# Kernel optimization log

Measured on AMD Instinct MI355X. Metric: run time of the kernel, lower is better.

The kernel has to match this reference:

```python
import jax, jax.numpy as jnp
import numpy as np

N, C, H_IMG, W_IMG = 32, 3, 224, 224
P = 14                      # number_patches per side
PH, PW = H_IMG // P, W_IMG // P
IN_DIM = C * PH * PW        # 768
D = 768                     # hidden_dimension
NH = 12                     # number_heads
DH = D // NH                # 64
L = 12                      # number_blocks
OUT = 1000                  # output_dimension
S = P * P + 1               # 197 tokens (cls + patches)
MLP = 4 * D                 # mlp_ratio * d


def sinusoidal_pos_emb(s, d):
    # result[i][j] = sin(i / 10000^(j/d)) if j even else cos(i / 10000^((j-1)/d))
    i = np.arange(s, dtype=np.float64)[:, None]
    j = np.arange(d)[None, :]
    angle = i / (10000.0 ** ((j - (j % 2)) / float(d)))
    emb = np.where(j % 2 == 0, np.sin(angle), np.cos(angle))
    return jnp.asarray(emb, jnp.float32)


def setup_inputs() -> dict:
    key = jax.random.key(0)
    ks = jax.random.split(key, 12)
    f32 = jnp.float32
    p = {}
    p['images'] = jax.random.normal(ks[0], (N, C, H_IMG, W_IMG), f32)
    p['W_map'] = jax.random.normal(ks[1], (IN_DIM, D), f32) * 0.02
    p['b_map'] = jnp.zeros((D,), f32)
    p['class_token'] = jax.random.normal(ks[2], (1, D), f32)
    p['pos_emb'] = sinusoidal_pos_emb(S, D)  # frozen (requires_grad=False)
    p['ln1_g'] = jnp.ones((L, D), f32)
    p['ln1_b'] = jnp.zeros((L, D), f32)
    p['Wq'] = jax.random.normal(ks[3], (L, NH, DH, DH), f32) * 0.02
    p['bq'] = jnp.zeros((L, NH, DH), f32)
    p['Wk'] = jax.random.normal(ks[4], (L, NH, DH, DH), f32) * 0.02
    p['bk'] = jnp.zeros((L, NH, DH), f32)
    p['Wv'] = jax.random.normal(ks[5], (L, NH, DH, DH), f32) * 0.02
    p['bv'] = jnp.zeros((L, NH, DH), f32)
    p['ln2_g'] = jnp.ones((L, D), f32)
    p['ln2_b'] = jnp.zeros((L, D), f32)
    p['W1'] = jax.random.normal(ks[6], (L, D, MLP), f32) * 0.02
    p['b1'] = jnp.zeros((L, MLP), f32)
    p['W2'] = jax.random.normal(ks[7], (L, MLP, D), f32) * 0.02
    p['b2'] = jnp.zeros((L, D), f32)
    p['W_head'] = jax.random.normal(ks[8], (D, OUT), f32) * 0.02
    p['b_head'] = jnp.zeros((OUT,), f32)
    return p


def _layer_norm(x, g, b, eps=1e-5):
    mu = jnp.mean(x, axis=-1, keepdims=True)
    var = jnp.var(x, axis=-1, keepdims=True)
    return (x - mu) * jax.lax.rsqrt(var + eps) * g + b


def reference(images, W_map, b_map, class_token, pos_emb, ln1_g, ln1_b,
              Wq, bq, Wk, bk, Wv, bv, ln2_g, ln2_b, W1, b1, W2, b2,
              W_head, b_head):
    n = images.shape[0]
    # patchify: [N,C,H,W] -> [N, P*P, C*ph*pw]; per-patch flatten is (C,ph,pw) order
    patches = images.reshape(n, C, P, PH, P, PW)
    patches = patches.transpose(0, 2, 4, 1, 3, 5).reshape(n, P * P, IN_DIM)
    tokens = patches @ W_map + b_map                         # [N, P*P, D]
    cls = jnp.broadcast_to(class_token[None], (n, 1, D))
    x = jnp.concatenate([cls, tokens], axis=1) + pos_emb     # [N, S, D]

    scale = DH ** 0.5
    for l in range(L):
        # --- MHSA with per-head independent Linear weights ---
        h = _layer_norm(x, ln1_g[l], ln1_b[l])
        xh = h.reshape(n, S, NH, DH)
        q = jnp.einsum('nshd,hde->nshe', xh, Wq[l]) + bq[l]
        k = jnp.einsum('nshd,hde->nshe', xh, Wk[l]) + bk[l]
        v = jnp.einsum('nshd,hde->nshe', xh, Wv[l]) + bv[l]
        scores = jnp.einsum('nqhd,nkhd->nhqk', q, k) / scale  # [N,H,S,S]
        attn = jax.nn.softmax(scores, axis=-1)
        o = jnp.einsum('nhqk,nkhd->nqhd', attn, v).reshape(n, S, D)
        x = x + o
        # --- MLP (exact GELU, as torch.nn.GELU default) ---
        h2 = _layer_norm(x, ln2_g[l], ln2_b[l])
        m = jax.nn.gelu(h2 @ W1[l] + b1[l], approximate=False) @ W2[l] + b2[l]
        x = x + m

    logits = x[:, 0] @ W_head + b_head
    return jax.nn.softmax(logits, axis=-1)
```

## Files before the change

kernel.cpp:

```cpp
#include <hip/hip_runtime.h>
#include <hip/hip_bf16.h>

constexpr int N_   = 32;
constexpr int C_   = 3;
constexpr int P_   = 14;
constexpr int PHW  = 16;
constexpr int IND  = 768;
constexpr int D_   = 768;
constexpr int NH_  = 12;
constexpr int DH_  = 64;
constexpr int L_   = 12;
constexpr int OUT_ = 1000;
constexpr int S_   = 197;
constexpr int MLP_ = 3072;
constexpr int NPATCH = P_ * P_;
constexpr int ROWS   = N_ * S_;
constexpr int TROWS  = N_ * NPATCH;
constexpr int RPAD   = 6400;
constexpr int SP_R   = 256;
constexpr int SP_C   = 224;

typedef __attribute__((ext_vector_type(8))) short bf16x8;
typedef __attribute__((ext_vector_type(4))) float f32x4;

__device__ __forceinline__ float bf2f(ushort u) {
    union { float f; unsigned int i; } v; v.i = ((unsigned int)u) << 16; return v.f;
}
__device__ __forceinline__ ushort f2bf(float f) {
    union { float f; unsigned int i; } v; v.f = f;
    unsigned int r = v.i + 0x7fffu + ((v.i >> 16) & 1u);
    return (ushort)(r >> 16);
}

__global__ __launch_bounds__(256)
void mfma_gemm(const ushort* __restrict__ Ag,
               const ushort* __restrict__ Bg,
               void* __restrict__ Cg,
               const float* __restrict__ bias,
               int M, int N, int K,
               int lda, int ldb, int ldc,
               long offA1, long offA2,
               long offB1, long offB2,
               long offC1, long offC2,
               int inner, float alpha, int act, int outbf, int accum)
{
    const int bz = blockIdx.z;
    const int bi = bz / inner, bj = bz % inner;
    const ushort* A = Ag + bi * offA1 + bj * offA2;
    const ushort* B = Bg + bi * offB1 + bj * offB2;
    const long coff = bi * offC1 + bj * offC2;

    __shared__ ushort As[128 * 32];
    __shared__ ushort Bs[128 * 32];

    const int tid  = threadIdx.x;
    const int w    = tid >> 6;
    const int lhi  = (tid & 63) >> 4;
    const int llo  = tid & 15;
    const int wr   = w >> 1, wc = w & 1;
    const int row0 = blockIdx.y * 128;
    const int col0 = blockIdx.x * 128;

    f32x4 acc[4][4];
#pragma unroll
    for (int m = 0; m < 4; ++m)
#pragma unroll
        for (int n = 0; n < 4; ++n) acc[m][n] = (f32x4){0.f, 0.f, 0.f, 0.f};

    int r0s = (0 * 256 + tid) >> 2, s0s = tid & 3;
    int r1s = (1 * 256 + tid) >> 2, s1s = tid & 3;
    int ss0 = s0s ^ ((r0s >> 1) & 3);
    int ss1 = s1s ^ ((r1s >> 1) & 3);
    ushort* dstA0 = As + ((0 * 256 + (w << 6)) << 3);
    ushort* dstA1 = As + ((1 * 256 + (w << 6)) << 3);
    ushort* dstB0 = Bs + ((0 * 256 + (w << 6)) << 3);
    ushort* dstB1 = Bs + ((1 * 256 + (w << 6)) << 3);

    for (int k0 = 0; k0 < K; k0 += 32) {
        const ushort* a0 = A + (long)(row0 + r0s) * lda + k0 + ss0 * 8;
        const ushort* a1 = A + (long)(row0 + r1s) * lda + k0 + ss1 * 8;
        const ushort* b0 = B + (long)(col0 + r0s) * ldb + k0 + ss0 * 8;
        const ushort* b1 = B + (long)(col0 + r1s) * ldb + k0 + ss1 * 8;
        __builtin_amdgcn_global_load_lds((const __attribute__((address_space(1))) void*)a0,
                                         (__attribute__((address_space(3))) void*)dstA0, 16, 0, 0);
        __builtin_amdgcn_global_load_lds((const __attribute__((address_space(1))) void*)a1,
                                         (__attribute__((address_space(3))) void*)dstA1, 16, 0, 0);
        __builtin_amdgcn_global_load_lds((const __attribute__((address_space(1))) void*)b0,
                                         (__attribute__((address_space(3))) void*)dstB0, 16, 0, 0);
        __builtin_amdgcn_global_load_lds((const __attribute__((address_space(1))) void*)b1,
                                         (__attribute__((address_space(3))) void*)dstB1, 16, 0, 0);
        __syncthreads();

        bf16x8 av[4], bv[4];
#pragma unroll
        for (int m = 0; m < 4; ++m) {
            int R = wr * 64 + m * 16 + llo;
            av[m] = *(const bf16x8*)(As + R * 32 + ((lhi ^ ((R >> 1) & 3)) << 3));
        }
#pragma unroll
        for (int n = 0; n < 4; ++n) {
            int R = wc * 64 + n * 16 + llo;
            bv[n] = *(const bf16x8*)(Bs + R * 32 + ((lhi ^ ((R >> 1) & 3)) << 3));
        }
#pragma unroll
        for (int m = 0; m < 4; ++m)
#pragma unroll
            for (int n = 0; n < 4; ++n)
                acc[m][n] = __builtin_amdgcn_mfma_f32_16x16x32_bf16(av[m], bv[n], acc[m][n], 0, 0, 0);
        __syncthreads();
    }

    float* Cf = (float*)Cg + coff;
    ushort* Ch = (ushort*)Cg + coff;
#pragma unroll
    for (int m = 0; m < 4; ++m) {
#pragma unroll
        for (int n = 0; n < 4; ++n) {
#pragma unroll
            for (int j = 0; j < 4; ++j) {
                int gr = row0 + wr * 64 + m * 16 + lhi * 4 + j;
                int gc = col0 + wc * 64 + n * 16 + llo;
                if (gr < M && gc < N) {
                    float v = acc[m][n][j] * alpha;
                    if (bias) v += bias[gc];
                    if (act == 1) v = 0.5f * v * (1.f + erff(v * 0.70710678118654752f));
                    long ci = (long)gr * ldc + gc;
                    if (outbf) {
                        Ch[ci] = f2bf(v);
                    } else {
                        if (accum) v += Cf[ci];
                        Cf[ci] = v;
                    }
                }
            }
        }
    }
}

__global__ __launch_bounds__(256)
void im2col_kernel(const float* __restrict__ img, ushort* __restrict__ patches)
{
    long idx = (long)blockIdx.x * 256 + threadIdx.x;
    if (idx >= (long)TROWS * IND) return;
    int e = (int)(idx % IND);
    int t = (int)((idx / IND) % NPATCH);
    int n = (int)(idx / ((long)IND * NPATCH));
    int pw = e & 15, ph = (e >> 4) & 15, c = e >> 8;
    int px = t % P_, py = t / P_;
    patches[idx] = f2bf(img[(((long)n * C_ + c) * 224 + py * PHW + ph) * 224 + px * PHW + pw]);
}

__global__ __launch_bounds__(256)
void assemble_kernel(const float* __restrict__ tokens,
                     const float* __restrict__ cls,
                     const float* __restrict__ pos,
                     float* __restrict__ x)
{
    long idx = (long)blockIdx.x * 256 + threadIdx.x;
    if (idx >= (long)ROWS * D_) return;
    int d = (int)(idx % D_);
    int s = (int)((idx / D_) % S_);
    long n = idx / ((long)D_ * S_);
    float v = (s == 0) ? cls[d] : tokens[((long)n * NPATCH + (s - 1)) * D_ + d];
    x[idx] = v + pos[(long)s * D_ + d];
}

__global__ __launch_bounds__(256)
void layernorm_kernel(const float* __restrict__ x, ushort* __restrict__ out,
                      const float* __restrict__ g, const float* __restrict__ b)
{
    long row = blockIdx.x;
    const float* xr = x + row * D_;
    ushort* orow = out + row * D_;
    int tid = threadIdx.x;
    float v0 = xr[tid], v1 = xr[tid + 256], v2 = xr[tid + 512];
    float s  = v0 + v1 + v2;
    float sq = v0 * v0 + v1 * v1 + v2 * v2;
    for (int off = 32; off > 0; off >>= 1) {
        s  += __shfl_down(s, off);
        sq += __shfl_down(sq, off);
    }
    __shared__ float rs[4], rq[4];
    int wave = tid >> 6, lane = tid & 63;
    if (lane == 0) { rs[wave] = s; rq[wave] = sq; }
    __syncthreads();
    float S  = rs[0] + rs[1] + rs[2] + rs[3];
    float SQ = rq[0] + rq[1] + rq[2] + rq[3];
    float mean = S * (1.f / 768.f);
    float var  = SQ * (1.f / 768.f) - mean * mean;
    float rstd = rsqrtf(var + 1e-5f);
    orow[tid]       = f2bf((v0 - mean) * rstd * g[tid]       + b[tid]);
    orow[tid + 256] = f2bf((v1 - mean) * rstd * g[tid + 256] + b[tid + 256]);
    orow[tid + 512] = f2bf((v2 - mean) * rstd * g[tid + 512] + b[tid + 512]);
}

__global__ __launch_bounds__(64)
void softmax197_kernel(ushort* __restrict__ scores)
{
    long bid = blockIdx.x;
    long batch = bid / S_;
    long r = bid % S_;
    ushort* p = scores + (batch * SP_R + r) * SP_C;
    int lane = threadIdx.x;
    float v[4];
    float mx = -INFINITY;
#pragma unroll
    for (int i = 0; i < 4; ++i) {
        int idx = lane + i * 64;
        v[i] = (idx < S_) ? bf2f(p[idx]) : -INFINITY;
        mx = fmaxf(mx, v[i]);
    }
    for (int off = 32; off > 0; off >>= 1) mx = fmaxf(mx, __shfl_xor(mx, off));
    float sum = 0.f;
#pragma unroll
    for (int i = 0; i < 4; ++i) {
        int idx = lane + i * 64;
        if (idx < S_) { v[i] = expf(v[i] - mx); sum += v[i]; }
    }
    for (int off = 32; off > 0; off >>= 1) sum += __shfl_xor(sum, off);
    float inv = 1.f / sum;
#pragma unroll
    for (int i = 0; i < 4; ++i) {
        int idx = lane + i * 64;
        if (idx < SP_C) p[idx] = (idx < S_) ? f2bf(v[i] * inv) : (ushort)0;
    }
}

__global__ __launch_bounds__(256)
void vtrans_kernel(const ushort* __restrict__ qkv, ushort* __restrict__ Vt)
{
    int b = blockIdx.z;
    int n = b / NH_, h = b % NH_;
    __shared__ ushort t[32][33];
    int s0 = blockIdx.x * 32, d0 = blockIdx.y * 32;
    int tx = threadIdx.x & 31, ty = threadIdx.x >> 5;
#pragma unroll
    for (int i = 0; i < 4; ++i) {
        int s = s0 + ty * 4 + i;
        ushort v = 0;
        if (s < S_) v = qkv[(long)(n * S_ + s) * 2304 + 1536 + h * 64 + d0 + tx];
        t[ty * 4 + i][tx] = v;
    }
    __syncthreads();
#pragma unroll
    for (int i = 0; i < 4; ++i) {
        int dh = d0 + ty * 4 + i;
        int s  = s0 + tx;
        Vt[((long)b * 64 + dh) * SP_C + s] = t[tx][ty * 4 + i];
    }
}

__global__ __launch_bounds__(256)
void transcast_kernel(const float* __restrict__ in, ushort* __restrict__ out, int R, int C)
{
    __shared__ float t[32][33];
    int c0 = blockIdx.x * 32, r0 = blockIdx.y * 32;
    int tx = threadIdx.x & 31, ty = threadIdx.x >> 5;
#pragma unroll
    for (int i = 0; i < 4; ++i) {
        int r = r0 + ty * 4 + i, c = c0 + tx;
        float v = 0.f;
        if (r < R && c < C) v = in[(long)r * C + c];
        t[ty * 4 + i][tx] = v;
    }
    __syncthreads();
#pragma unroll
    for (int i = 0; i < 4; ++i) {
        int c = c0 + ty * 4 + i, r = r0 + tx;
        if (c < C && r < R) out[(long)c * R + r] = f2bf(t[tx][ty * 4 + i]);
    }
}

__global__ __launch_bounds__(256)
void build_wqkvt_kernel(const float* __restrict__ Wq, const float* __restrict__ Wk,
                        const float* __restrict__ Wv, int l, ushort* __restrict__ out)
{
    long idx = (long)blockIdx.x * 256 + threadIdx.x;
    if (idx >= (long)2304 * 768) return;
    int n = (int)(idx / 768), k = (int)(idx % 768);
    int sec = n / 768, hn = (n % 768) / 64, e = n % 64;
    const float* W = sec == 0 ? Wq : (sec == 1 ? Wk : Wv);
    float v = 0.f;
    int d = k - hn * 64;
    if (d >= 0 && d < 64) v = W[(((long)l * NH_ + hn) * 64 + d) * 64 + e];
    out[idx] = f2bf(v);
}

__global__ __launch_bounds__(256)
void build_bqkv_kernel(const float* __restrict__ bq, const float* __restrict__ bk,
                       const float* __restrict__ bv, int l, float* __restrict__ out)
{
    int n = blockIdx.x * 256 + threadIdx.x;
    if (n >= 2304) return;
    int sec = n / 768, h = (n % 768) / 64, e = n % 64;
    const float* b = sec == 0 ? bq : (sec == 1 ? bk : bv);
    out[n] = b[((long)l * NH_ + h) * 64 + e];
}

template<int BM, int BN, int BK, int TM, int TN>
__global__ __launch_bounds__((BM / TM) * (BN / TN))
void gemm_f32(const float* __restrict__ A, const float* __restrict__ B,
              float* __restrict__ C, const float* __restrict__ bias,
              int M, int N, int K, int lda, int ldb, int ldc)
{
    constexpr int THREADS = (BM / TM) * (BN / TN);
    __shared__ float As[BK][BM + 4];
    __shared__ float Bs[BK][BN + 4];
    const int tid = threadIdx.x;
    const int row0 = blockIdx.y * BM, col0 = blockIdx.x * BN;
    const int tr = tid / (BN / TN), tc = tid % (BN / TN);
    float acc[TM][TN];
#pragma unroll
    for (int i = 0; i < TM; ++i)
#pragma unroll
        for (int j = 0; j < TN; ++j) acc[i][j] = 0.f;
    for (int k0 = 0; k0 < K; k0 += BK) {
#pragma unroll
        for (int it = 0; it < (BM * BK) / THREADS; ++it) {
            int idx = it * THREADS + tid;
            int m = idx / BK, kk = idx % BK;
            int gr = row0 + m, gk = k0 + kk;
            As[kk][m] = (gr < M && gk < K) ? A[(long)gr * lda + gk] : 0.f;
        }
#pragma unroll
        for (int it = 0; it < (BK * BN) / THREADS; ++it) {
            int idx = it * THREADS + tid;
            int kk = idx / BN, nn = idx % BN;
            int gk = k0 + kk, gn = col0 + nn;
            Bs[kk][nn] = (gk < K && gn < N) ? B[(long)gk * ldb + gn] : 0.f;
        }
        __syncthreads();
#pragma unroll
        for (int kk = 0; kk < BK; ++kk) {
            float a[TM], b[TN];
#pragma unroll
            for (int i = 0; i < TM; ++i) a[i] = As[kk][tr * TM + i];
#pragma unroll
            for (int j = 0; j < TN; ++j) b[j] = Bs[kk][tc * TN + j];
#pragma unroll
            for (int i = 0; i < TM; ++i)
#pragma unroll
                for (int j = 0; j < TN; ++j) acc[i][j] = fmaf(a[i], b[j], acc[i][j]);
        }
        __syncthreads();
    }
#pragma unroll
    for (int i = 0; i < TM; ++i) {
        int gr = row0 + tr * TM + i;
        if (gr >= M) continue;
#pragma unroll
        for (int j = 0; j < TN; ++j) {
            int gn = col0 + tc * TN + j;
            if (gn >= N) continue;
            C[(long)gr * ldc + gn] = acc[i][j] + bias[gn];
        }
    }
}

__global__ __launch_bounds__(256)
void softmax_out_kernel(const float* __restrict__ logits, float* __restrict__ out)
{
    int row = blockIdx.x;
    int tid = threadIdx.x;
    const float* p = logits + (long)row * OUT_;
    float v[4];
    float mx = -INFINITY;
#pragma unroll
    for (int i = 0; i < 4; ++i) {
        int idx = tid + i * 256;
        v[i] = (idx < OUT_) ? p[idx] : -INFINITY;
        mx = fmaxf(mx, v[i]);
    }
    int wave = tid >> 6, lane = tid & 63;
    for (int off = 32; off > 0; off >>= 1) mx = fmaxf(mx, __shfl_xor(mx, off));
    __shared__ float r1[4], r2[4];
    if (lane == 0) r1[wave] = mx;
    __syncthreads();
    mx = fmaxf(fmaxf(r1[0], r1[1]), fmaxf(r1[2], r1[3]));
    float sum = 0.f;
#pragma unroll
    for (int i = 0; i < 4; ++i) {
        int idx = tid + i * 256;
        if (idx < OUT_) { v[i] = expf(v[i] - mx); sum += v[i]; }
    }
    for (int off = 32; off > 0; off >>= 1) sum += __shfl_xor(sum, off);
    if (lane == 0) r2[wave] = sum;
    __syncthreads();
    sum = r2[0] + r2[1] + r2[2] + r2[3];
    float inv = 1.f / sum;
#pragma unroll
    for (int i = 0; i < 4; ++i) {
        int idx = tid + i * 256;
        if (idx < OUT_) out[(long)row * OUT_ + idx] = v[i] * inv;
    }
}

extern "C" void kernel_launch(void* const* d_in, const int* in_sizes, int n_in,
                              void* d_out, int out_size, void* d_ws, size_t ws_size,
                              hipStream_t stream)
{
    const float* images = (const float*)d_in[0];
    const float* W_map  = (const float*)d_in[1];
    const float* b_map  = (const float*)d_in[2];
    const float* cls    = (const float*)d_in[3];
    const float* pos    = (const float*)d_in[4];
    const float* ln1_g  = (const float*)d_in[5];
    const float* ln1_b  = (const float*)d_in[6];
    const float* Wq     = (const float*)d_in[7];
    const float* bq     = (const float*)d_in[8];
    const float* Wk     = (const float*)d_in[9];
    const float* bk     = (const float*)d_in[10];
    const float* Wv     = (const float*)d_in[11];
    const float* bv     = (const float*)d_in[12];
    const float* ln2_g  = (const float*)d_in[13];
    const float* ln2_b  = (const float*)d_in[14];
    const float* W1     = (const float*)d_in[15];
    const float* b1     = (const float*)d_in[16];
    const float* W2     = (const float*)d_in[17];
    const float* b2     = (const float*)d_in[18];
    const float* W_head = (const float*)d_in[19];
    const float* b_head = (const float*)d_in[20];

    char* base = (char*)d_ws;
    float*  x       = (float*)base;   base += (long)RPAD * D_ * 4;
    ushort* hbuf    = (ushort*)base;  base += (long)RPAD * D_ * 2;
    ushort* qkv     = (ushort*)base;  base += (long)RPAD * 2304 * 2;
    ushort* Vt      = (ushort*)base;  base += (long)385 * 64 * SP_C * 2;
    ushort* scoresP = (ushort*)base;  base += (long)384 * SP_R * SP_C * 2;
    ushort* mbuf    = (ushort*)base;  base += (long)RPAD * MLP_ * 2;
    ushort* Wmapt   = (ushort*)base;  base += (long)D_ * IND * 2;
    ushort* Wqkvt   = (ushort*)base;  base += (long)2304 * 768 * 2;
    float*  bqkv    = (float*)base;   base += (long)2304 * 4;
    ushort* W1t     = (ushort*)base;  base += (long)MLP_ * D_ * 2;
    ushort* W2t     = (ushort*)base;  base += (long)D_ * MLP_ * 2;
    float*  logits  = (float*)base;   base += (long)N_ * OUT_ * 4;

    float*  tokens  = (float*)scoresP;
    ushort* patches = mbuf;

    transcast_kernel<<<dim3((D_ + 31) / 32, (IND + 31) / 32), 256, 0, stream>>>(W_map, Wmapt, IND, D_);
    {
        long tot = (long)TROWS * IND;
        im2col_kernel<<<(int)((tot + 255) / 256), 256, 0, stream>>>(images, patches);
    }
    mfma_gemm<<<dim3(D_ / 128, TROWS / 128, 1), 256, 0, stream>>>(
        patches, Wmapt, tokens, b_map,
        TROWS, D_, IND, IND, IND, D_,
        0L, 0L, 0L, 0L, 0L, 0L, 1, 1.f, 0, 0, 0);
    {
        long tot = (long)ROWS * D_;
        assemble_kernel<<<(int)((tot + 255) / 256), 256, 0, stream>>>(tokens, cls, pos, x);
    }

    for (int l = 0; l < L_; ++l) {
        layernorm_kernel<<<ROWS, 256, 0, stream>>>(x, hbuf, ln1_g + (long)l * D_, ln1_b + (long)l * D_);

        build_wqkvt_kernel<<<(2304 * 768 + 255) / 256, 256, 0, stream>>>(Wq, Wk, Wv, l, Wqkvt);
        build_bqkv_kernel<<<(2304 + 255) / 256, 256, 0, stream>>>(bq, bk, bv, l, bqkv);

        mfma_gemm<<<dim3(2304 / 128, RPAD / 128, 1), 256, 0, stream>>>(
            hbuf, Wqkvt, qkv, bqkv,
            ROWS, 2304, D_, D_, D_, 2304,
            0L, 0L, 0L, 0L, 0L, 0L, 1, 1.f, 0, 1, 0);

        vtrans_kernel<<<dim3((S_ + 31) / 32, 2, N_ * NH_), 256, 0, stream>>>(qkv, Vt);

        mfma_gemm<<<dim3(2, 2, N_ * NH_), 256, 0, stream>>>(
            qkv, qkv + 768, scoresP, nullptr,
            S_, S_, DH_, 2304, 2304, SP_C,
            (long)S_ * 2304, 64L, (long)S_ * 2304, 64L,
            (long)NH_ * SP_R * SP_C, (long)SP_R * SP_C,
            NH_, 0.125f, 0, 1, 0);

        softmax197_kernel<<<N_ * NH_ * S_, 64, 0, stream>>>(scoresP);

        mfma_gemm<<<dim3(1, 2, N_ * NH_), 256, 0, stream>>>(
            scoresP, Vt, x, nullptr,
            S_, DH_, SP_C, SP_C, SP_C, D_,
            (long)NH_ * SP_R * SP_C, (long)SP_R * SP_C,
            (long)NH_ * 64 * SP_C, (long)64 * SP_C,
            (long)S_ * D_, 64L,
            NH_, 1.f, 0, 0, 1);

        layernorm_kernel<<<ROWS, 256, 0, stream>>>(x, hbuf, ln2_g + (long)l * D_, ln2_b + (long)l * D_);

        transcast_kernel<<<dim3((MLP_ + 31) / 32, (D_ + 31) / 32), 256, 0, stream>>>(
            W1 + (long)l * D_ * MLP_, W1t, D_, MLP_);
        mfma_gemm<<<dim3(MLP_ / 128, RPAD / 128, 1), 256, 0, stream>>>(
            hbuf, W1t, mbuf, b1 + (long)l * MLP_,
            ROWS, MLP_, D_, D_, D_, MLP_,
            0L, 0L, 0L, 0L, 0L, 0L, 1, 1.f, 1, 1, 0);

        transcast_kernel<<<dim3((D_ + 31) / 32, (MLP_ + 31) / 32), 256, 0, stream>>>(
            W2 + (long)l * MLP_ * D_, W2t, MLP_, D_);
        mfma_gemm<<<dim3(D_ / 128, RPAD / 128, 1), 256, 0, stream>>>(
            mbuf, W2t, x, b2 + (long)l * D_,
            ROWS, D_, MLP_, MLP_, MLP_, D_,
            0L, 0L, 0L, 0L, 0L, 0L, 1, 1.f, 0, 0, 1);
    }

    gemm_f32<64, 64, 16, 4, 4><<<dim3((OUT_ + 63) / 64, 1, 1), 256, 0, stream>>>(
        x, W_head, logits, b_head, N_, OUT_, D_, S_ * D_, OUT_, OUT_);
    softmax_out_kernel<<<N_, 256, 0, stream>>>(logits, (float*)d_out);
}
```

Before: 5.028 ms.

## Batch per-head QKV GEMM, hoist weight prep out of layer loop, rework head

The dense block-diagonal QKV GEMM (2304x768, mostly zeros) is replaced by a grouped GEMM over 36 small 64x64 per-head projections, so zero blocks are no longer multiplied. It adds per-group bias offsets to the GEMM kernel. All per-layer weight transposes and casts (QKV, W1, W2, biases) are hoisted before the loop when the workspace is large enough, falling back to per-layer casts otherwise. Softmax packs four rows per 256-thread block, and the f32 classifier GEMM is replaced by a transpose plus a wave-per-logit dot-product kernel. The grouped QKV GEMM uses K=64 tiles with N=64 inside 128-wide tiles, so MFMA utilisation may be low.

```diff
diff --git a/kernel.cpp b/kernel.cpp
--- a/kernel.cpp
+++ b/kernel.cpp
@@ -36,12 +36,13 @@
 void mfma_gemm(const ushort* __restrict__ Ag,
                const ushort* __restrict__ Bg,
                void* __restrict__ Cg,
-               const float* __restrict__ bias,
+               const float* __restrict__ biasg,
                int M, int N, int K,
                int lda, int ldb, int ldc,
                long offA1, long offA2,
                long offB1, long offB2,
                long offC1, long offC2,
+               long offS1, long offS2,
                int inner, float alpha, int act, int outbf, int accum)
 {
     const int bz = blockIdx.z;
@@ -49,6 +50,7 @@
     const ushort* A = Ag + bi * offA1 + bj * offA2;
     const ushort* B = Bg + bi * offB1 + bj * offB2;
     const long coff = bi * offC1 + bj * offC2;
+    const float* bias = biasg ? (biasg + bi * offS1 + bj * offS2) : nullptr;
 
     __shared__ ushort As[128 * 32];
     __shared__ ushort Bs[128 * 32];
@@ -194,14 +196,15 @@
     orow[tid + 512] = f2bf((v2 - mean) * rstd * g[tid + 512] + b[tid + 512]);
 }
 
-__global__ __launch_bounds__(64)
+__global__ __launch_bounds__(256)
 void softmax197_kernel(ushort* __restrict__ scores)
 {
-    long bid = blockIdx.x;
-    long batch = bid / S_;
-    long r = bid % S_;
+    long rid = (long)blockIdx.x * 4 + (threadIdx.x >> 6);
+    if (rid >= (long)N_ * NH_ * S_) return;
+    long batch = rid / S_;
+    long r = rid % S_;
     ushort* p = scores + (batch * SP_R + r) * SP_C;
-    int lane = threadIdx.x;
+    int lane = threadIdx.x & 63;
     float v[4];
     float mx = -INFINITY;
 #pragma unroll
@@ -251,7 +254,31 @@
 }
 
 __global__ __launch_bounds__(256)
-void transcast_kernel(const float* __restrict__ in, ushort* __restrict__ out, int R, int C)
+void transcast_kernel(const float* __restrict__ in, ushort* __restrict__ out,
+                      int R, int C, long inL, long outL)
+{
+    const float* ip = in + (long)blockIdx.z * inL;
+    ushort* op = out + (long)blockIdx.z * outL;
+    __shared__ float t[32][33];
+    int c0 = blockIdx.x * 32, r0 = blockIdx.y * 32;
+    int tx = threadIdx.x & 31, ty = threadIdx.x >> 5;
+#pragma unroll
+    for (int i = 0; i < 4; ++i) {
+        int r = r0 + ty * 4 + i, c = c0 + tx;
+        float v = 0.f;
+        if (r < R && c < C) v = ip[(long)r * C + c];
+        t[ty * 4 + i][tx] = v;
+    }
+    __syncthreads();
+#pragma unroll
+    for (int i = 0; i < 4; ++i) {
+        int c = c0 + ty * 4 + i, r = r0 + tx;
+        if (c < C && r < R) op[(long)c * R + r] = f2bf(t[tx][ty * 4 + i]);
+    }
+}
+
+__global__ __launch_bounds__(256)
+void transf32_kernel(const float* __restrict__ in, float* __restrict__ out, int R, int C)
 {
     __shared__ float t[32][33];
     int c0 = blockIdx.x * 32, r0 = blockIdx.y * 32;
@@ -267,94 +294,51 @@
 #pragma unroll
     for (int i = 0; i < 4; ++i) {
         int c = c0 + ty * 4 + i, r = r0 + tx;
-        if (c < C && r < R) out[(long)c * R + r] = f2bf(t[tx][ty * 4 + i]);
-    }
-}
-
-__global__ __launch_bounds__(256)
-void build_wqkvt_kernel(const float* __restrict__ Wq, const float* __restrict__ Wk,
-                        const float* __restrict__ Wv, int l, ushort* __restrict__ out)
+        if (c < C && r < R) out[(long)c * R + r] = t[tx][ty * 4 + i];
+    }
+}
+
+__global__ __launch_bounds__(256)
+void build_wqkvC_kernel(const float* __restrict__ Wq, const float* __restrict__ Wk,
+                        const float* __restrict__ Wv, int l0, ushort* __restrict__ out)
 {
     long idx = (long)blockIdx.x * 256 + threadIdx.x;
-    if (idx >= (long)2304 * 768) return;
-    int n = (int)(idx / 768), k = (int)(idx % 768);
-    int sec = n / 768, hn = (n % 768) / 64, e = n % 64;
+    if (idx >= 36L * 4096) return;
+    int z = blockIdx.z, l = l0 + z;
+    int sec = (int)(idx / 49152);
+    int r   = (int)(idx % 49152);
+    int h = r / 4096, rr = r % 4096, e = rr / 64, d = rr % 64;
     const float* W = sec == 0 ? Wq : (sec == 1 ? Wk : Wv);
-    float v = 0.f;
-    int d = k - hn * 64;
-    if (d >= 0 && d < 64) v = W[(((long)l * NH_ + hn) * 64 + d) * 64 + e];
-    out[idx] = f2bf(v);
+    out[(long)z * 147456 + idx] = f2bf(W[(((long)l * NH_ + h) * 64 + d) * 64 + e]);
 }
 
 __global__ __launch_bounds__(256)
 void build_bqkv_kernel(const float* __restrict__ bq, const float* __restrict__ bk,
-                       const float* __restrict__ bv, int l, float* __restrict__ out)
-{
-    int n = blockIdx.x * 256 + threadIdx.x;
-    if (n >= 2304) return;
+                       const float* __restrict__ bv, float* __restrict__ out)
+{
+    int i = blockIdx.x * 256 + threadIdx.x;
+    if (i >= L_ * 2304) return;
+    int l = i / 2304, n = i % 2304;
     int sec = n / 768, h = (n % 768) / 64, e = n % 64;
     const float* b = sec == 0 ? bq : (sec == 1 ? bk : bv);
-    out[n] = b[((long)l * NH_ + h) * 64 + e];
-}
-
-template<int BM, int BN, int BK, int TM, int TN>
-__global__ __launch_bounds__((BM / TM) * (BN / TN))
-void gemm_f32(const float* __restrict__ A, const float* __restrict__ B,
-              float* __restrict__ C, const float* __restrict__ bias,
-              int M, int N, int K, int lda, int ldb, int ldc)
-{
-    constexpr int THREADS = (BM / TM) * (BN / TN);
-    __shared__ float As[BK][BM + 4];
-    __shared__ float Bs[BK][BN + 4];
-    const int tid = threadIdx.x;
-    const int row0 = blockIdx.y * BM, col0 = blockIdx.x * BN;
-    const int tr = tid / (BN / TN), tc = tid % (BN / TN);
-    float acc[TM][TN];
-#pragma unroll
-    for (int i = 0; i < TM; ++i)
-#pragma unroll
-        for (int j = 0; j < TN; ++j) acc[i][j] = 0.f;
-    for (int k0 = 0; k0 < K; k0 += BK) {
-#pragma unroll
-        for (int it = 0; it < (BM * BK) / THREADS; ++it) {
-            int idx = it * THREADS + tid;
-            int m = idx / BK, kk = idx % BK;
-            int gr = row0 + m, gk = k0 + kk;
-            As[kk][m] = (gr < M && gk < K) ? A[(long)gr * lda + gk] : 0.f;
-        }
-#pragma unroll
-        for (int it = 0; it < (BK * BN) / THREADS; ++it) {
-            int idx = it * THREADS + tid;
-            int kk = idx / BN, nn = idx % BN;
-            int gk = k0 + kk, gn = col0 + nn;
-            Bs[kk][nn] = (gk < K && gn < N) ? B[(long)gk * ldb + gn] : 0.f;
-        }
-        __syncthreads();
-#pragma unroll
-        for (int kk = 0; kk < BK; ++kk) {
-            float a[TM], b[TN];
-#pragma unroll
-            for (int i = 0; i < TM; ++i) a[i] = As[kk][tr * TM + i];
-#pragma unroll
-            for (int j = 0; j < TN; ++j) b[j] = Bs[kk][tc * TN + j];
-#pragma unroll
-            for (int i = 0; i < TM; ++i)
-#pragma unroll
-                for (int j = 0; j < TN; ++j) acc[i][j] = fmaf(a[i], b[j], acc[i][j]);
-        }
-        __syncthreads();
-    }
-#pragma unroll
-    for (int i = 0; i < TM; ++i) {
-        int gr = row0 + tr * TM + i;
-        if (gr >= M) continue;
-#pragma unroll
-        for (int j = 0; j < TN; ++j) {
-            int gn = col0 + tc * TN + j;
-            if (gn >= N) continue;
-            C[(long)gr * ldc + gn] = acc[i][j] + bias[gn];
-        }
-    }
+    out[i] = b[((long)l * NH_ + h) * 64 + e];
+}
+
+__global__ __launch_bounds__(256)
+void head_kernel(const float* __restrict__ x, const float* __restrict__ Wt,
+                 const float* __restrict__ bhead, float* __restrict__ logits)
+{
+    int wid = blockIdx.x * 4 + (threadIdx.x >> 6);
+    int lane = threadIdx.x & 63;
+    int n = wid / OUT_, c = wid % OUT_;
+    if (n >= N_) return;
+    const float* xr = x + (long)n * S_ * D_;
+    const float* wr = Wt + (long)c * D_;
+    float acc = 0.f;
+#pragma unroll
+    for (int i = 0; i < 12; ++i) acc += xr[lane + i * 64] * wr[lane + i * 64];
+    for (int off = 32; off > 0; off >>= 1) acc += __shfl_down(acc, off);
+    if (lane == 0) logits[(long)n * OUT_ + c] = acc + bhead[c];
 }
 
 __global__ __launch_bounds__(256)
@@ -422,23 +406,40 @@
     const float* b_head = (const float*)d_in[20];
 
     char* base = (char*)d_ws;
-    float*  x       = (float*)base;   base += (long)RPAD * D_ * 4;
-    ushort* hbuf    = (ushort*)base;  base += (long)RPAD * D_ * 2;
-    ushort* qkv     = (ushort*)base;  base += (long)RPAD * 2304 * 2;
-    ushort* Vt      = (ushort*)base;  base += (long)385 * 64 * SP_C * 2;
-    ushort* scoresP = (ushort*)base;  base += (long)384 * SP_R * SP_C * 2;
-    ushort* mbuf    = (ushort*)base;  base += (long)RPAD * MLP_ * 2;
-    ushort* Wmapt   = (ushort*)base;  base += (long)D_ * IND * 2;
-    ushort* Wqkvt   = (ushort*)base;  base += (long)2304 * 768 * 2;
-    float*  bqkv    = (float*)base;   base += (long)2304 * 4;
-    ushort* W1t     = (ushort*)base;  base += (long)MLP_ * D_ * 2;
-    ushort* W2t     = (ushort*)base;  base += (long)D_ * MLP_ * 2;
-    float*  logits  = (float*)base;   base += (long)N_ * OUT_ * 4;
-
+    float*  x       = (float*)base;   base += 19660800L;
+    ushort* hbuf    = (ushort*)base;  base += 9830400L;
+    ushort* qkv     = (ushort*)base;  base += 29491200L;
+    ushort* Vt      = (ushort*)base;  base += 11038720L;
+    ushort* scoresP = (ushort*)base;  base += 44040192L;
+    ushort* mbuf    = (ushort*)base;  base += 39321600L;
+    ushort* Wmapt   = (ushort*)base;  base += 1179648L;
+    float*  bqkvA   = (float*)base;   base += 110592L;
+    ushort* WqkvC   = (ushort*)base;  base += 3538944L;
+
+    size_t used = (size_t)(base - (char*)d_ws);
+    const long W1L_ALL = 56623104L, W2L_ALL = 56623104L;
+    const long W1L_ONE = 4718592L,  W2L_ONE = 4718592L;
+    bool hoist = ws_size >= used + (size_t)(W1L_ALL + W2L_ALL);
+    ushort* W1tA = (ushort*)base;  base += hoist ? W1L_ALL : W1L_ONE;
+    ushort* W2tA = (ushort*)base;  base += hoist ? W2L_ALL : W2L_ONE;
+    const long w1str = hoist ? 3072L * 768 : 0;
+    const long w2str = hoist ? 768L * 3072 : 0;
+
+    float* W_headT = (float*)scoresP;
+    float* logits  = (float*)((char*)scoresP + 3072000L);
     float*  tokens  = (float*)scoresP;
     ushort* patches = mbuf;
 
-    transcast_kernel<<<dim3((D_ + 31) / 32, (IND + 31) / 32), 256, 0, stream>>>(W_map, Wmapt, IND, D_);
+    build_wqkvC_kernel<<<dim3(576, 1, L_), 256, 0, stream>>>(Wq, Wk, Wv, 0, WqkvC);
+    build_bqkv_kernel<<<(L_ * 2304 + 255) / 256, 256, 0, stream>>>(bq, bk, bv, bqkvA);
+    transcast_kernel<<<dim3(24, 24, 1), 256, 0, stream>>>(W_map, Wmapt, IND, D_, 0L, 0L);
+    if (hoist) {
+        transcast_kernel<<<dim3(96, 24, L_), 256, 0, stream>>>(W1, W1tA, D_, MLP_,
+                                                               (long)D_ * MLP_, 3072L * 768);
+        transcast_kernel<<<dim3(24, 96, L_), 256, 0, stream>>>(W2, W2tA, MLP_, D_,
+                                                               (long)MLP_ * D_, 768L * 3072);
+    }
+
     {
         long tot = (long)TROWS * IND;
         im2col_kernel<<<(int)((tot + 255) / 256), 256, 0, stream>>>(images, patches);
@@ -446,7 +447,7 @@
     mfma_gemm<<<dim3(D_ / 128, TROWS / 128, 1), 256, 0, stream>>>(
         patches, Wmapt, tokens, b_map,
         TROWS, D_, IND, IND, IND, D_,
-        0L, 0L, 0L, 0L, 0L, 0L, 1, 1.f, 0, 0, 0);
+        0L, 0L, 0L, 0L, 0L, 0L, 0L, 0L, 1, 1.f, 0, 0, 0);
     {
         long tot = (long)ROWS * D_;
         assemble_kernel<<<(int)((tot + 255) / 256), 256, 0, stream>>>(tokens, cls, pos, x);
@@ -455,51 +456,54 @@
     for (int l = 0; l < L_; ++l) {
         layernorm_kernel<<<ROWS, 256, 0, stream>>>(x, hbuf, ln1_g + (long)l * D_, ln1_b + (long)l * D_);
 
-        build_wqkvt_kernel<<<(2304 * 768 + 255) / 256, 256, 0, stream>>>(Wq, Wk, Wv, l, Wqkvt);
-        build_bqkv_kernel<<<(2304 + 255) / 256, 256, 0, stream>>>(bq, bk, bv, l, bqkv);
-
-        mfma_gemm<<<dim3(2304 / 128, RPAD / 128, 1), 256, 0, stream>>>(
-            hbuf, Wqkvt, qkv, bqkv,
-            ROWS, 2304, D_, D_, D_, 2304,
-            0L, 0L, 0L, 0L, 0L, 0L, 1, 1.f, 0, 1, 0);
-
-        vtrans_kernel<<<dim3((S_ + 31) / 32, 2, N_ * NH_), 256, 0, stream>>>(qkv, Vt);
+        mfma_gemm<<<dim3(1, RPAD / 128, 36), 256, 0, stream>>>(
+            hbuf, WqkvC + (long)l * 147456, qkv, bqkvA + (long)l * 2304,
+            ROWS, 64, 64, D_, 64, 2304,
+            0L, 64L,
+            12L * 4096, 4096L,
+            768L, 64L,
+            768L, 64L,
+            12, 1.f, 0, 1, 0);
+
+        vtrans_kernel<<<dim3(7, 2, N_ * NH_), 256, 0, stream>>>(qkv, Vt);
 
         mfma_gemm<<<dim3(2, 2, N_ * NH_), 256, 0, stream>>>(
             qkv, qkv + 768, scoresP, nullptr,
             S_, S_, DH_, 2304, 2304, SP_C,
             (long)S_ * 2304, 64L, (long)S_ * 2304, 64L,
-            (long)NH_ * SP_R * SP_C, (long)SP_R * SP_C,
+            (long)NH_ * SP_R * SP_C, (long)SP_R * SP_C, 0L, 0L,
             NH_, 0.125f, 0, 1, 0);
 
-        softmax197_kernel<<<N_ * NH_ * S_, 64, 0, stream>>>(scoresP);
+        softmax197_kernel<<<(N_ * NH_ * S_ + 3) / 4, 256, 0, stream>>>(scoresP);
 
         mfma_gemm<<<dim3(1, 2, N_ * NH_), 256, 0, stream>>>(
             scoresP, Vt, x, nullptr,
             S_, DH_, SP_C, SP_C, SP_C, D_,
             (long)NH_ * SP_R * SP_C, (long)SP_R * SP_C,
             (long)NH_ * 64 * SP_C, (long)64 * SP_C,
-            (long)S_ * D_, 64L,
+            (long)S_ * D_, 64L, 0L, 0L,
             NH_, 1.f, 0, 0, 1);
 
         layernorm_kernel<<<ROWS, 256, 0, stream>>>(x, hbuf, ln2_g + (long)l * D_, ln2_b + (long)l * D_);
 
-        transcast_kernel<<<dim3((MLP_ + 31) / 32, (D_ + 31) / 32), 256, 0, stream>>>(
-            W1 + (long)l * D_ * MLP_, W1t, D_, MLP_);
+        if (!hoist)
+            transcast_kernel<<<dim3(96, 24, 1), 256, 0, stream>>>(
+                W1 + (long)l * D_ * MLP_, W1tA, D_, MLP_, 0L, 0L);
         mfma_gemm<<<dim3(MLP_ / 128, RPAD / 128, 1), 256, 0, stream>>>(
-            hbuf, W1t, mbuf, b1 + (long)l * MLP_,
+            hbuf, W1tA + (long)l * w1str, mbuf, b1 + (long)l * MLP_,
             ROWS, MLP_, D_, D_, D_, MLP_,
-            0L, 0L, 0L, 0L, 0L, 0L, 1, 1.f, 1, 1, 0);
-
-        transcast_kernel<<<dim3((D_ + 31) / 32, (MLP_ + 31) / 32), 256, 0, stream>>>(
-            W2 + (long)l * MLP_ * D_, W2t, MLP_, D_);
+            0L, 0L, 0L, 0L, 0L, 0L, 0L, 0L, 1, 1.f, 1, 1, 0);
+
+        if (!hoist)
+            transcast_kernel<<<dim3(24, 96, 1), 256, 0, stream>>>(
+                W2 + (long)l * MLP_ * D_, W2tA, MLP_, D_, 0L, 0L);
         mfma_gemm<<<dim3(D_ / 128, RPAD / 128, 1), 256, 0, stream>>>(
-            mbuf, W2t, x, b2 + (long)l * D_,
+            mbuf, W2tA + (long)l * w2str, x, b2 + (long)l * D_,
             ROWS, D_, MLP_, MLP_, MLP_, D_,
-            0L, 0L, 0L, 0L, 0L, 0L, 1, 1.f, 0, 0, 1);
-    }
-
-    gemm_f32<64, 64, 16, 4, 4><<<dim3((OUT_ + 63) / 64, 1, 1), 256, 0, stream>>>(
-        x, W_head, logits, b_head, N_, OUT_, D_, S_ * D_, OUT_, OUT_);
+            0L, 0L, 0L, 0L, 0L, 0L, 0L, 0L, 1, 1.f, 0, 0, 1);
+    }
+
+    transf32_kernel<<<dim3(32, 24), 256, 0, stream>>>(W_head, W_headT, D_, OUT_);
+    head_kernel<<<(N_ * OUT_) / 4, 256, 0, stream>>>(x, W_headT, b_head, logits);
     softmax_out_kernel<<<N_, 256, 0, stream>>>(logits, (float*)d_out);
 }
```

After: 4.472 ms. 1.12x faster.
